# Kernel tuning notes

Measured on AMD Instinct MI355X. Metric: run time of the kernel, lower is better.

The kernel has to match this reference:

```python
import jax, jax.numpy as jnp
import numpy as np
from math import pi as PI, log

B, N, D, K = 16, 16384, 64, 64


def setup_inputs() -> dict:
    key = jax.random.key(0)
    k1, k2, k3, k4 = jax.random.split(key, 4)
    x = jax.random.normal(k1, (B, N, D), dtype=jnp.float32)
    pi_w = jax.nn.softmax(jax.random.normal(k2, (K,), dtype=jnp.float32))  # mixture weights, sum to 1
    mu = jax.random.normal(k3, (K, D), dtype=jnp.float32)
    var = jax.random.uniform(k4, (K, D), dtype=jnp.float32, minval=0.5, maxval=1.5)  # diagonal variances
    return {"x": x, "pi": pi_w, "mu": mu, "var": var}


def reference(x, pi, mu, var):
    b, n, d = x.shape
    # --- gmm.predict_proba: diagonal-covariance Gaussian log-likelihoods + log pi, softmax over K ---
    inv_var = 1.0 / var                                   # (K, D)
    x2 = x * x                                            # (B, N, D)
    # Mahalanobis distance expanded via matmuls to avoid a (B,N,K,D) intermediate
    maha = (jnp.einsum('bnd,kd->bnk', x2, inv_var)
            - 2.0 * jnp.einsum('bnd,kd->bnk', x, mu * inv_var)
            + jnp.sum(mu * mu * inv_var, axis=-1))        # (B, N, K)
    log_det = jnp.sum(jnp.log(var), axis=-1)              # (K,)
    log_prob = -0.5 * (d * log(2.0 * PI) + log_det + maha)
    Q = jax.nn.softmax(log_prob + jnp.log(pi), axis=-1)   # (B, N, K) responsibilities
    # --- weighted reductions over N ---
    Q_sum = jnp.sum(Q, axis=1) / n                         # (B, K)
    Q_x = jnp.einsum('bnk,bnd->bkd', Q, x) / n             # (B, K, D)
    Q_x2 = jnp.einsum('bnk,bnd->bkd', Q, x2) / n           # (B, K, D)
    # --- Fisher-vector statistics ---
    d_pi = Q_sum - pi                                      # (B, K)
    qs = Q_sum[..., None]                                  # (B, K, 1)
    d_mu = Q_x - qs * mu
    d_sigma = -Q_x2 - qs * (mu * mu) + qs * var + 2.0 * Q_x * mu
    return jnp.concatenate([d_pi.reshape(b, -1), d_mu.reshape(b, -1), d_sigma.reshape(b, -1)], axis=1)
```

## Files before the change

### kernel.cpp

```cpp
#include <hip/hip_runtime.h>
#include <math.h>

#define B_  16
#define N_  16384
#define D_  64
#define K_  64
#define OUT_PER_B (K_ + 2*K_*D_)
#define PART_FLOATS OUT_PER_B

#define WS_C0_OFF   4096
#define WS_PART_OFF 4160

typedef float f32x4 __attribute__((ext_vector_type(4)));
typedef short short8 __attribute__((ext_vector_type(8)));

__device__ __forceinline__ unsigned short f2bf(float f) {
    union { float f; unsigned int u; } v; v.f = f;
    unsigned int r = v.u + 0x7FFFu + ((v.u >> 16) & 1u);
    return (unsigned short)(r >> 16);
}

__global__ __launch_bounds__(256) void fv_prep(const float* __restrict__ pi,
                                               const float* __restrict__ mu,
                                               const float* __restrict__ var,
                                               float* __restrict__ ws) {
    int t = threadIdx.x;
    unsigned short* wt = (unsigned short*)ws;
    for (int i = t; i < 4096; i += 256) {
        int k = i >> 6, d = i & 63;
        float v  = var[i];
        float m  = mu[i];
        float iv = 1.0f / v;
        wt[k * 128 + d]      = f2bf(-0.5f * iv);
        wt[k * 128 + 64 + d] = f2bf(m * iv);
    }
    if (t < 64) {
        float s = 0.0f;
        for (int d = 0; d < 64; ++d) {
            float v = var[t * 64 + d];
            float m = mu[t * 64 + d];
            s += logf(v) + m * m / v;
        }
        ws[WS_C0_OFF + t] = logf(pi[t]) - 0.5f * (117.624132f + s);
    }
}

__global__ __launch_bounds__(256, 4) void fv_main(const float* __restrict__ x,
                                                  const float* __restrict__ ws,
                                                  float* __restrict__ partials,
                                                  int chunks) {
    __shared__ __align__(16) unsigned short WtS[64 * 136];
    __shared__ __align__(16) unsigned short QtS[64 * 72];
    __shared__ float c0s[64];
    __shared__ float qsum_s[4][64];

    const int t    = threadIdx.x;
    const int w    = t >> 6;
    const int lane = t & 63;
    const int r16  = lane & 15;
    const int q    = lane >> 4;

    {
        const uint4* src = (const uint4*)ws;
        for (int i = t; i < 1024; i += 256) {
            int row = i >> 4, u = i & 15;
            *(uint4*)&WtS[row * 136 + u * 8] = src[i];
        }
        if (t < 64) c0s[t] = ws[WS_C0_OFF + t];
    }

    const int bi    = blockIdx.y;
    const int chunk = blockIdx.x;
    const int ppb   = N_ / chunks;
    const float* xb = x + ((size_t)bi * N_ + (size_t)chunk * ppb) * D_;

    f32x4 accX[4]  = {};
    f32x4 accX2[4] = {};
    float qsacc[4][4] = {};

    __syncthreads();

    const int ntiles = ppb / 64;
    for (int tile = 0; tile < ntiles; ++tile) {
        const float* xt = xb + (size_t)tile * 64 * D_;

        const float* xrow = xt + (16 * w + r16) * D_ + 8 * q;
        float4 va = *(const float4*)(xrow);
        float4 vb = *(const float4*)(xrow + 4);
        float4 vc = *(const float4*)(xrow + 32);
        float4 vd = *(const float4*)(xrow + 36);

        short8 fxa, fxb, fx2a, fx2b;
        {
            const float* pa = &va.x; const float* pb = &vb.x;
            const float* pc = &vc.x; const float* pd = &vd.x;
            #pragma unroll
            for (int j = 0; j < 4; ++j) {
                fxa[j]      = (short)f2bf(pa[j]);
                fxa[j + 4]  = (short)f2bf(pb[j]);
                fxb[j]      = (short)f2bf(pc[j]);
                fxb[j + 4]  = (short)f2bf(pd[j]);
                fx2a[j]     = (short)f2bf(pa[j] * pa[j]);
                fx2a[j + 4] = (short)f2bf(pb[j] * pb[j]);
                fx2b[j]     = (short)f2bf(pc[j] * pc[j]);
                fx2b[j + 4] = (short)f2bf(pd[j] * pd[j]);
            }
        }

        float sc[4][4];
        #pragma unroll
        for (int kt = 0; kt < 4; ++kt) {
            f32x4 a;
            a[0] = c0s[16 * kt + 4 * q + 0];
            a[1] = c0s[16 * kt + 4 * q + 1];
            a[2] = c0s[16 * kt + 4 * q + 2];
            a[3] = c0s[16 * kt + 4 * q + 3];
            const unsigned short* wr = &WtS[(16 * kt + r16) * 136 + 8 * q];
            a = __builtin_amdgcn_mfma_f32_16x16x32_bf16(*(const short8*)(const void*)(wr),      fx2a, a, 0, 0, 0);
            a = __builtin_amdgcn_mfma_f32_16x16x32_bf16(*(const short8*)(const void*)(wr + 32), fx2b, a, 0, 0, 0);
            a = __builtin_amdgcn_mfma_f32_16x16x32_bf16(*(const short8*)(const void*)(wr + 64), fxa,  a, 0, 0, 0);
            a = __builtin_amdgcn_mfma_f32_16x16x32_bf16(*(const short8*)(const void*)(wr + 96), fxb,  a, 0, 0, 0);
            sc[kt][0] = a[0]; sc[kt][1] = a[1]; sc[kt][2] = a[2]; sc[kt][3] = a[3];
        }

        float mx = sc[0][0];
        #pragma unroll
        for (int kt = 0; kt < 4; ++kt)
            #pragma unroll
            for (int rr = 0; rr < 4; ++rr) mx = fmaxf(mx, sc[kt][rr]);
        mx = fmaxf(mx, __shfl_xor(mx, 16));
        mx = fmaxf(mx, __shfl_xor(mx, 32));
        float z = 0.0f;
        #pragma unroll
        for (int kt = 0; kt < 4; ++kt)
            #pragma unroll
            for (int rr = 0; rr < 4; ++rr) {
                sc[kt][rr] = __expf(sc[kt][rr] - mx);
                z += sc[kt][rr];
            }
        z += __shfl_xor(z, 16);
        z += __shfl_xor(z, 32);
        float inv = 1.0f / z;
        const int p = 16 * w + r16;
        #pragma unroll
        for (int kt = 0; kt < 4; ++kt)
            #pragma unroll
            for (int rr = 0; rr < 4; ++rr) {
                float qv = sc[kt][rr] * inv;
                qsacc[kt][rr] += qv;
                QtS[(16 * kt + 4 * q + rr) * 72 + p] = f2bf(qv);
            }
        __syncthreads();

        const int d = 16 * w + r16;
        const float* xcol = xt + d;
        float vle[2][8];
        #pragma unroll
        for (int c = 0; c < 2; ++c)
            #pragma unroll
            for (int j = 0; j < 8; ++j)
                vle[c][j] = xcol[(32 * c + 8 * q + j) * D_];
        short8 fxp[2], fx2p[2];
        #pragma unroll
        for (int c = 0; c < 2; ++c)
            #pragma unroll
            for (int j = 0; j < 8; ++j) {
                float v = vle[c][j];
                fxp[c][j]  = (short)f2bf(v);
                fx2p[c][j] = (short)f2bf(v * v);
            }
        #pragma unroll
        for (int kt = 0; kt < 4; ++kt) {
            const unsigned short* qr = &QtS[(16 * kt + r16) * 72 + 8 * q];
            short8 aq0 = *(const short8*)(const void*)(qr);
            short8 aq1 = *(const short8*)(const void*)(qr + 32);
            accX[kt]  = __builtin_amdgcn_mfma_f32_16x16x32_bf16(aq0, fxp[0],  accX[kt],  0, 0, 0);
            accX2[kt] = __builtin_amdgcn_mfma_f32_16x16x32_bf16(aq0, fx2p[0], accX2[kt], 0, 0, 0);
            accX[kt]  = __builtin_amdgcn_mfma_f32_16x16x32_bf16(aq1, fxp[1],  accX[kt],  0, 0, 0);
            accX2[kt] = __builtin_amdgcn_mfma_f32_16x16x32_bf16(aq1, fx2p[1], accX2[kt], 0, 0, 0);
        }
        __syncthreads();
    }

    float* part = partials + ((size_t)bi * chunks + chunk) * PART_FLOATS;
    #pragma unroll
    for (int kt = 0; kt < 4; ++kt)
        #pragma unroll
        for (int rr = 0; rr < 4; ++rr) {
            int k = 16 * kt + 4 * q + rr;
            part[64 + k * 64 + 16 * w + r16]        = accX[kt][rr];
            part[64 + 4096 + k * 64 + 16 * w + r16] = accX2[kt][rr];
        }
    #pragma unroll
    for (int kt = 0; kt < 4; ++kt)
        #pragma unroll
        for (int rr = 0; rr < 4; ++rr) {
            float v = qsacc[kt][rr];
            v += __shfl_xor(v, 1);
            v += __shfl_xor(v, 2);
            v += __shfl_xor(v, 4);
            v += __shfl_xor(v, 8);
            if (r16 == 0) qsum_s[w][16 * kt + 4 * q + rr] = v;
        }
    __syncthreads();
    if (t < 64)
        part[t] = qsum_s[0][t] + qsum_s[1][t] + qsum_s[2][t] + qsum_s[3][t];
}

__global__ __launch_bounds__(256) void fv_finalize(const float* __restrict__ pi,
                                                   const float* __restrict__ mu,
                                                   const float* __restrict__ var,
                                                   const float* __restrict__ partials,
                                                   float* __restrict__ out,
                                                   int chunks) {
    int g = blockIdx.x * 256 + threadIdx.x;
    if (g >= B_ * OUT_PER_B) return;
    int b   = g / OUT_PER_B;
    int pos = g - b * OUT_PER_B;
    const float* base = partials + (size_t)b * chunks * PART_FLOATS;
    const float invN = 1.0f / (float)N_;

    if (pos < 64) {
        float qs = 0.0f;
        for (int c = 0; c < chunks; ++c) qs += base[c * PART_FLOATS + pos];
        out[g] = qs * invN - pi[pos];
    } else if (pos < 64 + 4096) {
        int idx = pos - 64;
        int k = idx >> 6;
        float qs = 0.0f, qx = 0.0f;
        for (int c = 0; c < chunks; ++c) {
            qs += base[c * PART_FLOATS + k];
            qx += base[c * PART_FLOATS + pos];
        }
        out[g] = (qx - qs * mu[idx]) * invN;
    } else {
        int idx = pos - 64 - 4096;
        int k = idx >> 6;
        float qs = 0.0f, qx = 0.0f, qx2 = 0.0f;
        for (int c = 0; c < chunks; ++c) {
            qs  += base[c * PART_FLOATS + k];
            qx  += base[c * PART_FLOATS + 64 + idx];
            qx2 += base[c * PART_FLOATS + pos];
        }
        float m = mu[idx], v = var[idx];
        out[g] = (-qx2 - qs * m * m + qs * v + 2.0f * qx * m) * invN;
    }
}

extern "C" void kernel_launch(void* const* d_in, const int* in_sizes, int n_in,
                              void* d_out, int out_size, void* d_ws, size_t ws_size,
                              hipStream_t stream) {
    const float* x   = (const float*)d_in[0];
    const float* pi  = (const float*)d_in[1];
    const float* mu  = (const float*)d_in[2];
    const float* var = (const float*)d_in[3];
    float* ws = (float*)d_ws;

    int chunks = 64;
    while (chunks > 1 &&
           (size_t)(WS_PART_OFF + (size_t)B_ * chunks * PART_FLOATS) * sizeof(float) > ws_size)
        chunks >>= 1;
    float* partials = ws + WS_PART_OFF;

    fv_prep<<<1, 256, 0, stream>>>(pi, mu, var, ws);
    fv_main<<<dim3(chunks, B_), 256, 0, stream>>>(x, ws, partials, chunks);
    int total = B_ * OUT_PER_B;
    fv_finalize<<<(total + 255) / 256, 256, 0, stream>>>(pi, mu, var, partials,
                                                         (float*)d_out, chunks);
}
```

Measured before the change: 142.3 us.

## Keep GMM weight fragments in registers, pack bf16 conversions, halve chunk count

Loads the per-component weight MFMA fragments and constant offsets straight into registers once, removing the shared-memory weight tile and its initial barrier. Converts fp32 to bf16 two values at a time with the packed intrinsic, and issues the column loads for the second GEMM before the barrier so their latency overlaps the wait. Launch bounds drop to 2 blocks per SIMD to make room for the extra registers, and the chunk count falls from 64 to 32, giving fewer partials to reduce but also fewer blocks in flight.

Measured after the change: 134.5 us. -5.5%, faster.

```diff
diff --git a/kernel.cpp b/kernel.cpp
--- a/kernel.cpp
+++ b/kernel.cpp
@@ -1,4 +1,5 @@
 #include <hip/hip_runtime.h>
+#include <hip/hip_bf16.h>
 #include <math.h>
 
 #define B_  16
@@ -7,17 +8,27 @@
 #define K_  64
 #define OUT_PER_B (K_ + 2*K_*D_)
 #define PART_FLOATS OUT_PER_B
+#define CHUNKS 32
 
 #define WS_C0_OFF   4096
 #define WS_PART_OFF 4160
 
 typedef float f32x4 __attribute__((ext_vector_type(4)));
 typedef short short8 __attribute__((ext_vector_type(8)));
+
+union U8 { short8 s8; unsigned int u[4]; };
 
 __device__ __forceinline__ unsigned short f2bf(float f) {
     union { float f; unsigned int u; } v; v.f = f;
     unsigned int r = v.u + 0x7FFFu + ((v.u >> 16) & 1u);
     return (unsigned short)(r >> 16);
+}
+
+__device__ __forceinline__ unsigned int f2bf2(float lo, float hi) {
+    __hip_bfloat162 h = __float22bfloat162_rn(make_float2(lo, hi));
+    unsigned int u;
+    __builtin_memcpy(&u, &h, 4);
+    return u;
 }
 
 __global__ __launch_bounds__(256) void fv_prep(const float* __restrict__ pi,
@@ -45,13 +56,11 @@
     }
 }
 
-__global__ __launch_bounds__(256, 4) void fv_main(const float* __restrict__ x,
+__global__ __launch_bounds__(256, 2) void fv_main(const float* __restrict__ x,
                                                   const float* __restrict__ ws,
                                                   float* __restrict__ partials,
                                                   int chunks) {
-    __shared__ __align__(16) unsigned short WtS[64 * 136];
     __shared__ __align__(16) unsigned short QtS[64 * 72];
-    __shared__ float c0s[64];
     __shared__ float qsum_s[4][64];
 
     const int t    = threadIdx.x;
@@ -60,13 +69,18 @@
     const int r16  = lane & 15;
     const int q    = lane >> 4;
 
+    short8 wfrag[4][4];
+    f32x4  c0v[4];
     {
-        const uint4* src = (const uint4*)ws;
-        for (int i = t; i < 1024; i += 256) {
-            int row = i >> 4, u = i & 15;
-            *(uint4*)&WtS[row * 136 + u * 8] = src[i];
-        }
-        if (t < 64) c0s[t] = ws[WS_C0_OFF + t];
+        const unsigned short* wsu = (const unsigned short*)ws;
+        #pragma unroll
+        for (int kt = 0; kt < 4; ++kt) {
+            const unsigned short* wr = wsu + (16 * kt + r16) * 128 + 8 * q;
+            #pragma unroll
+            for (int h = 0; h < 4; ++h)
+                wfrag[kt][h] = *(const short8*)(const void*)(wr + 32 * h);
+            c0v[kt] = *(const f32x4*)(ws + WS_C0_OFF + 16 * kt + 4 * q);
+        }
     }
 
     const int bi    = blockIdx.y;
@@ -77,8 +91,6 @@
     f32x4 accX[4]  = {};
     f32x4 accX2[4] = {};
     float qsacc[4][4] = {};
-
-    __syncthreads();
 
     const int ntiles = ppb / 64;
     for (int tile = 0; tile < ntiles; ++tile) {
@@ -90,36 +102,24 @@
         float4 vc = *(const float4*)(xrow + 32);
         float4 vd = *(const float4*)(xrow + 36);
 
-        short8 fxa, fxb, fx2a, fx2b;
-        {
-            const float* pa = &va.x; const float* pb = &vb.x;
-            const float* pc = &vc.x; const float* pd = &vd.x;
-            #pragma unroll
-            for (int j = 0; j < 4; ++j) {
-                fxa[j]      = (short)f2bf(pa[j]);
-                fxa[j + 4]  = (short)f2bf(pb[j]);
-                fxb[j]      = (short)f2bf(pc[j]);
-                fxb[j + 4]  = (short)f2bf(pd[j]);
-                fx2a[j]     = (short)f2bf(pa[j] * pa[j]);
-                fx2a[j + 4] = (short)f2bf(pb[j] * pb[j]);
-                fx2b[j]     = (short)f2bf(pc[j] * pc[j]);
-                fx2b[j + 4] = (short)f2bf(pd[j] * pd[j]);
-            }
-        }
+        U8 fxa, fxb, fx2a, fx2b;
+        fxa.u[0]  = f2bf2(va.x, va.y);           fxa.u[1]  = f2bf2(va.z, va.w);
+        fxa.u[2]  = f2bf2(vb.x, vb.y);           fxa.u[3]  = f2bf2(vb.z, vb.w);
+        fxb.u[0]  = f2bf2(vc.x, vc.y);           fxb.u[1]  = f2bf2(vc.z, vc.w);
+        fxb.u[2]  = f2bf2(vd.x, vd.y);           fxb.u[3]  = f2bf2(vd.z, vd.w);
+        fx2a.u[0] = f2bf2(va.x*va.x, va.y*va.y); fx2a.u[1] = f2bf2(va.z*va.z, va.w*va.w);
+        fx2a.u[2] = f2bf2(vb.x*vb.x, vb.y*vb.y); fx2a.u[3] = f2bf2(vb.z*vb.z, vb.w*vb.w);
+        fx2b.u[0] = f2bf2(vc.x*vc.x, vc.y*vc.y); fx2b.u[1] = f2bf2(vc.z*vc.z, vc.w*vc.w);
+        fx2b.u[2] = f2bf2(vd.x*vd.x, vd.y*vd.y); fx2b.u[3] = f2bf2(vd.z*vd.z, vd.w*vd.w);
 
         float sc[4][4];
         #pragma unroll
         for (int kt = 0; kt < 4; ++kt) {
-            f32x4 a;
-            a[0] = c0s[16 * kt + 4 * q + 0];
-            a[1] = c0s[16 * kt + 4 * q + 1];
-            a[2] = c0s[16 * kt + 4 * q + 2];
-            a[3] = c0s[16 * kt + 4 * q + 3];
-            const unsigned short* wr = &WtS[(16 * kt + r16) * 136 + 8 * q];
-            a = __builtin_amdgcn_mfma_f32_16x16x32_bf16(*(const short8*)(const void*)(wr),      fx2a, a, 0, 0, 0);
-            a = __builtin_amdgcn_mfma_f32_16x16x32_bf16(*(const short8*)(const void*)(wr + 32), fx2b, a, 0, 0, 0);
-            a = __builtin_amdgcn_mfma_f32_16x16x32_bf16(*(const short8*)(const void*)(wr + 64), fxa,  a, 0, 0, 0);
-            a = __builtin_amdgcn_mfma_f32_16x16x32_bf16(*(const short8*)(const void*)(wr + 96), fxb,  a, 0, 0, 0);
+            f32x4 a = c0v[kt];
+            a = __builtin_amdgcn_mfma_f32_16x16x32_bf16(wfrag[kt][0], fx2a.s8, a, 0, 0, 0);
+            a = __builtin_amdgcn_mfma_f32_16x16x32_bf16(wfrag[kt][1], fx2b.s8, a, 0, 0, 0);
+            a = __builtin_amdgcn_mfma_f32_16x16x32_bf16(wfrag[kt][2], fxa.s8,  a, 0, 0, 0);
+            a = __builtin_amdgcn_mfma_f32_16x16x32_bf16(wfrag[kt][3], fxb.s8,  a, 0, 0, 0);
             sc[kt][0] = a[0]; sc[kt][1] = a[1]; sc[kt][2] = a[2]; sc[kt][3] = a[3];
         }
 
@@ -143,41 +143,45 @@
         float inv = 1.0f / z;
         const int p = 16 * w + r16;
         #pragma unroll
-        for (int kt = 0; kt < 4; ++kt)
+        for (int kt = 0; kt < 4; ++kt) {
             #pragma unroll
             for (int rr = 0; rr < 4; ++rr) {
                 float qv = sc[kt][rr] * inv;
                 qsacc[kt][rr] += qv;
                 QtS[(16 * kt + 4 * q + rr) * 72 + p] = f2bf(qv);
             }
+        }
+
+        const int dcol = 16 * w + r16;
+        const float* xcol = xt + dcol;
+        float vle[16];
+        #pragma unroll
+        for (int c = 0; c < 2; ++c)
+            #pragma unroll
+            for (int j = 0; j < 8; ++j)
+                vle[8 * c + j] = xcol[(32 * c + 8 * q + j) * D_];
+
         __syncthreads();
 
-        const int d = 16 * w + r16;
-        const float* xcol = xt + d;
-        float vle[2][8];
-        #pragma unroll
-        for (int c = 0; c < 2; ++c)
-            #pragma unroll
-            for (int j = 0; j < 8; ++j)
-                vle[c][j] = xcol[(32 * c + 8 * q + j) * D_];
-        short8 fxp[2], fx2p[2];
-        #pragma unroll
-        for (int c = 0; c < 2; ++c)
-            #pragma unroll
-            for (int j = 0; j < 8; ++j) {
-                float v = vle[c][j];
-                fxp[c][j]  = (short)f2bf(v);
-                fx2p[c][j] = (short)f2bf(v * v);
-            }
+        U8 fxp0, fxp1, fx2p0, fx2p1;
+        #pragma unroll
+        for (int i = 0; i < 4; ++i) {
+            float a0 = vle[2 * i], a1 = vle[2 * i + 1];
+            float b0 = vle[8 + 2 * i], b1 = vle[8 + 2 * i + 1];
+            fxp0.u[i]  = f2bf2(a0, a1);
+            fxp1.u[i]  = f2bf2(b0, b1);
+            fx2p0.u[i] = f2bf2(a0 * a0, a1 * a1);
+            fx2p1.u[i] = f2bf2(b0 * b0, b1 * b1);
+        }
         #pragma unroll
         for (int kt = 0; kt < 4; ++kt) {
             const unsigned short* qr = &QtS[(16 * kt + r16) * 72 + 8 * q];
             short8 aq0 = *(const short8*)(const void*)(qr);
             short8 aq1 = *(const short8*)(const void*)(qr + 32);
-            accX[kt]  = __builtin_amdgcn_mfma_f32_16x16x32_bf16(aq0, fxp[0],  accX[kt],  0, 0, 0);
-            accX2[kt] = __builtin_amdgcn_mfma_f32_16x16x32_bf16(aq0, fx2p[0], accX2[kt], 0, 0, 0);
-            accX[kt]  = __builtin_amdgcn_mfma_f32_16x16x32_bf16(aq1, fxp[1],  accX[kt],  0, 0, 0);
-            accX2[kt] = __builtin_amdgcn_mfma_f32_16x16x32_bf16(aq1, fx2p[1], accX2[kt], 0, 0, 0);
+            accX[kt]  = __builtin_amdgcn_mfma_f32_16x16x32_bf16(aq0, fxp0.s8,  accX[kt],  0, 0, 0);
+            accX2[kt] = __builtin_amdgcn_mfma_f32_16x16x32_bf16(aq0, fx2p0.s8, accX2[kt], 0, 0, 0);
+            accX[kt]  = __builtin_amdgcn_mfma_f32_16x16x32_bf16(aq1, fxp1.s8,  accX[kt],  0, 0, 0);
+            accX2[kt] = __builtin_amdgcn_mfma_f32_16x16x32_bf16(aq1, fx2p1.s8, accX2[kt], 0, 0, 0);
         }
         __syncthreads();
     }
@@ -256,7 +260,7 @@
     const float* var = (const float*)d_in[3];
     float* ws = (float*)d_ws;
 
-    int chunks = 64;
+    int chunks = CHUNKS;
     while (chunks > 1 &&
            (size_t)(WS_PART_OFF + (size_t)B_ * chunks * PART_FLOATS) * sizeof(float) > ws_size)
         chunks >>= 1;
```
